# Performance work log

Measured on AMD Instinct MI355X. Metric: run time of the kernel, lower is better.

Reference implementation:

```python
import jax, jax.numpy as jnp
import numpy as np

B, C, T = 256, 1, 16384   # batch, input_channels, seq_len
H = C                      # hidden_size == input_channels in this module
OUT = 1                    # output_channels


def setup_inputs() -> dict:
    key = jax.random.key(0)
    ks = jax.random.split(key, 11)
    # PyTorch GRU/Linear init: uniform(-1/sqrt(H), 1/sqrt(H)); H=1 -> (-1, 1)
    u = lambda k, shape, s=1.0: jax.random.uniform(k, shape, jnp.float32, -s, s)
    s_lin = 1.0 / np.sqrt(2 * H).astype(np.float32)
    return {
        "x": jax.random.normal(ks[0], (B, C, T), jnp.float32),
        # layer 0: input size C, per direction [3H, C] / [3H, H] / [3H]
        "w_ih0": u(ks[1], (2, 3 * H, C)),
        "w_hh0": u(ks[2], (2, 3 * H, H)),
        "b_ih0": u(ks[3], (2, 3 * H)),
        "b_hh0": u(ks[4], (2, 3 * H)),
        # layers 1-2: input size 2H (bidirectional concat)
        "w_ih12": u(ks[5], (2, 2, 3 * H, 2 * H)),
        "w_hh12": u(ks[6], (2, 2, 3 * H, H)),
        "b_ih12": u(ks[7], (2, 2, 3 * H)),
        "b_hh12": u(ks[8], (2, 2, 3 * H)),
        # output projection Linear(2H -> OUT)
        "w_out": u(ks[9], (OUT, 2 * H), s_lin),
        "b_out": u(ks[10], (OUT,), s_lin),
    }


def _gru_dir(xs, w_ih, w_hh, b_ih, b_hh, reverse):
    """One GRU direction. xs: [T, B, in] -> ys: [T, B, H] (time-aligned)."""
    h0 = jnp.zeros((xs.shape[1], w_hh.shape[1]), xs.dtype)

    def step(h, x_t):
        gi = x_t @ w_ih.T + b_ih          # [B, 3H]
        gh = h @ w_hh.T + b_hh            # [B, 3H]
        ir, iz, inn = jnp.split(gi, 3, axis=-1)
        hr, hz, hn = jnp.split(gh, 3, axis=-1)
        r = jax.nn.sigmoid(ir + hr)
        z = jax.nn.sigmoid(iz + hz)
        n = jnp.tanh(inn + r * hn)
        h_new = (1.0 - z) * n + z * h
        return h_new, h_new

    _, ys = jax.lax.scan(step, h0, xs, reverse=reverse)
    return ys


def _bidir(xs, w_ih_f, w_hh_f, b_ih_f, b_hh_f, w_ih_b, w_hh_b, b_ih_b, b_hh_b):
    fwd = _gru_dir(xs, w_ih_f, w_hh_f, b_ih_f, b_hh_f, reverse=False)
    bwd = _gru_dir(xs, w_ih_b, w_hh_b, b_ih_b, b_hh_b, reverse=True)
    return jnp.concatenate([fwd, bwd], axis=-1)  # [T, B, 2H]


def reference(x, w_ih0, w_hh0, b_ih0, b_hh0, w_ih12, w_hh12, b_ih12, b_hh12, w_out, b_out):
    xs = jnp.transpose(x, (2, 0, 1))  # [B, C, T] -> [T, B, C]
    xs = _bidir(xs, w_ih0[0], w_hh0[0], b_ih0[0], b_hh0[0],
                w_ih0[1], w_hh0[1], b_ih0[1], b_hh0[1])
    for l in range(2):  # GRU layers 1 and 2 (structurally distinct weights)
        xs = _bidir(xs, w_ih12[l, 0], w_hh12[l, 0], b_ih12[l, 0], b_hh12[l, 0],
                    w_ih12[l, 1], w_hh12[l, 1], b_ih12[l, 1], b_hh12[l, 1])
    y = xs @ w_out.T + b_out          # [T, B, OUT]
    return jnp.transpose(y, (1, 2, 0))  # [B, OUT, T]
```

## Files before the change

### kernel.cpp

```cpp
#include <hip/hip_runtime.h>
#include <hip/hip_fp16.h>

#define T_LEN 16384
#define B_SZ  256
#define S_CH  256
#define CL    (T_LEN / S_CH)
#define HALO  32
#define SC    16

__device__ __forceinline__ float ex2(float x)  { return __builtin_amdgcn_exp2f(x); }
__device__ __forceinline__ float rcpf(float x) { return __builtin_amdgcn_rcpf(x); }

__device__ __forceinline__ float ld_cvt(const float* p)  { return *p; }
__device__ __forceinline__ float ld_cvt(const __half* p) { return __half2float(*p); }
__device__ __forceinline__ void  st_cvt(float* p, float v)  { *p = v; }
__device__ __forceinline__ void  st_cvt(__half* p, float v) { *p = __float2half_rn(v); }

__device__ __forceinline__ float gru_step(float h, float preR, float preZ, float preN,
                                          float UR, float UZ, float UN2, float DN2)
{
    float er  = ex2(fmaf(h, UR, preR));
    float ez  = ex2(fmaf(h, UZ, preZ));
    float r   = rcpf(1.0f + er);
    float z   = rcpf(1.0f + ez);
    float hn2 = fmaf(h, UN2, DN2);
    float en  = ex2(fmaf(r, hn2, preN));
    float n   = fmaf(-2.0f, rcpf(1.0f + en), 1.0f);
    float omz = 1.0f - z;
    float zh  = z * h;
    return fmaf(n, omz, zh);
}

template<bool REV>
__device__ void scan0(const float* __restrict__ x,
                      const float* __restrict__ wih, const float* __restrict__ whh,
                      const float* __restrict__ bih, const float* __restrict__ bhh,
                      __half* __restrict__ out, int b, int s)
{
    const int d = REV ? 1 : 0;
    const float L2E = 1.4426950408889634f;
    const float WR  = -L2E * wih[d*3+0];
    const float WZ  = -L2E * wih[d*3+1];
    const float WN  =  2.0f*L2E * wih[d*3+2];
    const float UR  = -L2E * whh[d*3+0];
    const float UZ  = -L2E * whh[d*3+1];
    const float UN2 =  2.0f*L2E * whh[d*3+2];
    const float CR  = -L2E * (bih[d*3+0] + bhh[d*3+0]);
    const float CZ  = -L2E * (bih[d*3+1] + bhh[d*3+1]);
    const float CN  =  2.0f*L2E * bih[d*3+2];
    const float DN2 =  2.0f*L2E * bhh[d*3+2];

    const int warm   = min(HALO, REV ? (T_LEN - (s + 1) * CL) : (s * CL));
    const int nsteps = warm + CL;
    const int t0     = REV ? ((s + 1) * CL - 1 + warm) : (s * CL - warm);

    const float* row = x + (size_t)b * T_LEN;
    __half* po = out + (REV ? B_SZ : 0) + b;

    float xA[SC], xB[SC];
    float h = 0.0f;

    auto LD = [&](float* F, int base) {
        const float4* p = (const float4*)(row + (REV ? (t0 - base - 15) : (t0 + base)));
        float4 v0 = p[0], v1 = p[1], v2 = p[2], v3 = p[3];
        float lin[16] = { v0.x,v0.y,v0.z,v0.w, v1.x,v1.y,v1.z,v1.w,
                          v2.x,v2.y,v2.z,v2.w, v3.x,v3.y,v3.z,v3.w };
        #pragma unroll
        for (int k = 0; k < 16; ++k) F[k] = REV ? lin[15 - k] : lin[k];
        __builtin_amdgcn_sched_barrier(0);
    };

    auto CS = [&](float* F, int base) {
        float ov[SC];
        #pragma unroll
        for (int k = 0; k < SC; ++k) {
            float xv = F[k];
            h = gru_step(h, fmaf(xv, WR, CR), fmaf(xv, WZ, CZ), fmaf(xv, WN, CN),
                         UR, UZ, UN2, DN2);
            ov[k] = h;
        }
        if (base >= warm) {
            #pragma unroll
            for (int k = 0; k < SC; ++k) {
                int t = REV ? (t0 - (base + k)) : (t0 + (base + k));
                st_cvt(po + t * (2 * B_SZ), ov[k]);
            }
        }
    };

    LD(xA, 0);
    const int nsup = nsteps / SC;
    for (int i = 0; i < nsup; i += 2) {
        LD(xB, min((i + 1) * SC, nsteps - SC));
        CS(xA, i * SC);
        LD(xA, min((i + 2) * SC, nsteps - SC));
        CS(xB, (i + 1) * SC);
    }
}

template<bool REV, typename TIN, typename TOUT>
__device__ void scan12(const TIN* __restrict__ in,
                       const float* __restrict__ wih, const float* __restrict__ whh,
                       const float* __restrict__ bih, const float* __restrict__ bhh,
                       TOUT* __restrict__ out, int b, int s)
{
    const int d = REV ? 1 : 0;
    const float L2E = 1.4426950408889634f;
    const float WR0 = -L2E * wih[(d*3+0)*2+0], WR1 = -L2E * wih[(d*3+0)*2+1];
    const float WZ0 = -L2E * wih[(d*3+1)*2+0], WZ1 = -L2E * wih[(d*3+1)*2+1];
    const float WN0 =  2.0f*L2E * wih[(d*3+2)*2+0], WN1 = 2.0f*L2E * wih[(d*3+2)*2+1];
    const float UR  = -L2E * whh[d*3+0];
    const float UZ  = -L2E * whh[d*3+1];
    const float UN2 =  2.0f*L2E * whh[d*3+2];
    const float CR  = -L2E * (bih[d*3+0] + bhh[d*3+0]);
    const float CZ  = -L2E * (bih[d*3+1] + bhh[d*3+1]);
    const float CN  =  2.0f*L2E * bih[d*3+2];
    const float DN2 =  2.0f*L2E * bhh[d*3+2];

    const int warm   = min(HALO, REV ? (T_LEN - (s + 1) * CL) : (s * CL));
    const int nsteps = warm + CL;
    const int t0     = REV ? ((s + 1) * CL - 1 + warm) : (s * CL - warm);

    const TIN* pf = in + b;
    const TIN* pg = in + B_SZ + b;
    TOUT* po = out + (REV ? B_SZ : 0) + b;

    float fA[SC], gA[SC], fB[SC], gB[SC];
    float h = 0.0f;

#define LD12(F, G, base_) { int base = (base_); \
    _Pragma("unroll") for (int k = 0; k < SC; ++k) { \
      int t = REV ? (t0 - (base + k)) : (t0 + (base + k)); \
      F[k] = ld_cvt(pf + t * (2 * B_SZ)); G[k] = ld_cvt(pg + t * (2 * B_SZ)); } \
    __builtin_amdgcn_sched_barrier(0); }

#define CS12(F, G, base_) { int base = (base_); float ov[SC]; \
    _Pragma("unroll") for (int k = 0; k < SC; ++k) { \
      float a = F[k], c = G[k]; \
      float pr = fmaf(a, WR0, fmaf(c, WR1, CR)); \
      float pz = fmaf(a, WZ0, fmaf(c, WZ1, CZ)); \
      float pn = fmaf(a, WN0, fmaf(c, WN1, CN)); \
      h = gru_step(h, pr, pz, pn, UR, UZ, UN2, DN2); ov[k] = h; } \
    if (base >= warm) { \
      _Pragma("unroll") for (int k = 0; k < SC; ++k) { \
        int t = REV ? (t0 - (base + k)) : (t0 + (base + k)); \
        st_cvt(po + t * (2 * B_SZ), ov[k]); } } }

    LD12(fA, gA, 0);
    const int nsup = nsteps / SC;
    for (int i = 0; i < nsup; i += 2) {
        LD12(fB, gB, min((i + 1) * SC, nsteps - SC));
        CS12(fA, gA, i * SC);
        LD12(fA, gA, min((i + 2) * SC, nsteps - SC));
        CS12(fB, gB, (i + 1) * SC);
    }
#undef LD12
#undef CS12
}

__device__ __forceinline__ void decode_blk(int blk, int tid, int& b, int& s, int& dir)
{
    int xcd = blk & 7;
    int j   = blk >> 3;
    int sl  = j & 31;
    int bg  = (j >> 5) & 3;
    dir     = j >> 7;
    s       = xcd * 32 + sl;
    b       = bg * 64 + tid;
}

__global__ void __launch_bounds__(64) k_scan0g(const float* __restrict__ x,
                                               const float* __restrict__ wih,
                                               const float* __restrict__ whh,
                                               const float* __restrict__ bih,
                                               const float* __restrict__ bhh,
                                               __half* __restrict__ out)
{
    int b, s, dir;
    decode_blk(blockIdx.x, threadIdx.x, b, s, dir);
    if (dir == 0) scan0<false>(x, wih, whh, bih, bhh, out, b, s);
    else          scan0<true >(x, wih, whh, bih, bhh, out, b, s);
}

__global__ void __launch_bounds__(64) k_scan1g(const __half* __restrict__ in,
                                               const float* __restrict__ wih,
                                               const float* __restrict__ whh,
                                               const float* __restrict__ bih,
                                               const float* __restrict__ bhh,
                                               __half* __restrict__ out)
{
    int b, s, dir;
    decode_blk(blockIdx.x, threadIdx.x, b, s, dir);
    if (dir == 0) scan12<false>(in, wih, whh, bih, bhh, out, b, s);
    else          scan12<true >(in, wih, whh, bih, bhh, out, b, s);
}

__global__ void __launch_bounds__(128) k2p(const __half* __restrict__ in,
        const float* __restrict__ wih, const float* __restrict__ whh,
        const float* __restrict__ bih, const float* __restrict__ bhh,
        const float* __restrict__ wo, const float* __restrict__ bo,
        float* __restrict__ y)
{
    __shared__ float tY[64][65];

    const int blk  = blockIdx.x;
    const int xcd  = blk & 7;
    const int jj   = blk >> 3;
    const int sl   = jj & 31;
    const int bg   = jj >> 5;
    const int s    = xcd * 32 + sl;
    const int lane = threadIdx.x & 63;
    const int w    = threadIdx.x >> 6;
    const int b    = bg * 64 + lane;
    const int sg   = w ? -1 : 1;
    const int t0   = s * CL;

    const int d = w;
    const float L2E = 1.4426950408889634f;
    const float WR0 = -L2E * wih[(d*3+0)*2+0], WR1 = -L2E * wih[(d*3+0)*2+1];
    const float WZ0 = -L2E * wih[(d*3+1)*2+0], WZ1 = -L2E * wih[(d*3+1)*2+1];
    const float WN0 =  2.0f*L2E * wih[(d*3+2)*2+0], WN1 = 2.0f*L2E * wih[(d*3+2)*2+1];
    const float UR  = -L2E * whh[d*3+0];
    const float UZ  = -L2E * whh[d*3+1];
    const float UN2 =  2.0f*L2E * whh[d*3+2];
    const float CR  = -L2E * (bih[d*3+0] + bhh[d*3+0]);
    const float CZ  = -L2E * (bih[d*3+1] + bhh[d*3+1]);
    const float CN  =  2.0f*L2E * bih[d*3+2];
    const float DN2 =  2.0f*L2E * bhh[d*3+2];

    const int warm   = w ? min(HALO, T_LEN - (t0 + CL)) : min(HALO, t0);
    const int tstart = w ? (t0 + CL - 1 + warm) : (t0 - warm);

    const __half* pf = in + b;
    const __half* pg = in + B_SZ + b;

    float fA[SC], gA[SC], fB[SC], gB[SC];
    float f[CL];
    float h = 0.0f;

#define LD2(F, G, base_) { int base = (base_); \
    _Pragma("unroll") for (int k = 0; k < SC; ++k) { \
      int t = tstart + sg * (base + k); \
      F[k] = __half2float(pf[t * (2 * B_SZ)]); \
      G[k] = __half2float(pg[t * (2 * B_SZ)]); } \
    __builtin_amdgcn_sched_barrier(0); }

#define CSB(F, G) { \
    _Pragma("unroll") for (int k = 0; k < SC; ++k) { \
      float a = F[k], c = G[k]; \
      float pr = fmaf(a, WR0, fmaf(c, WR1, CR)); \
      float pz = fmaf(a, WZ0, fmaf(c, WZ1, CZ)); \
      float pn = fmaf(a, WN0, fmaf(c, WN1, CN)); \
      h = gru_step(h, pr, pz, pn, UR, UZ, UN2, DN2); } }

#define CSS(F, G, Q) { \
    _Pragma("unroll") for (int k = 0; k < SC; ++k) { \
      float a = F[k], c = G[k]; \
      float pr = fmaf(a, WR0, fmaf(c, WR1, CR)); \
      float pz = fmaf(a, WZ0, fmaf(c, WZ1, CZ)); \
      float pn = fmaf(a, WN0, fmaf(c, WN1, CN)); \
      h = gru_step(h, pr, pz, pn, UR, UZ, UN2, DN2); \
      f[(Q) * SC + k] = h; } }

    LD2(fA, gA, 0);
    if (warm) {
        LD2(fB, gB, SC);      CSB(fA, gA);
        LD2(fA, gA, 2 * SC);  CSB(fB, gB);
    }
    LD2(fB, gB, warm + SC);      CSS(fA, gA, 0);
    LD2(fA, gA, warm + 2 * SC);  CSS(fB, gB, 1);
    LD2(fB, gB, warm + 3 * SC);  CSS(fA, gA, 2);
                                 CSS(fB, gB, 3);
#undef LD2
#undef CSB
#undef CSS

    const float wf = wo[0], wb = wo[1], bias = bo[0];
    if (w == 0) {
        #pragma unroll
        for (int m = 0; m < CL; ++m) tY[lane][m] = fmaf(wf, f[m], bias);
    }
    __syncthreads();
    if (w == 1) {
        #pragma unroll
        for (int m = 0; m < CL; ++m) tY[lane][CL - 1 - m] += wb * f[m];
    }
    __syncthreads();
    {
        const int b0 = bg * 64;
        const int c4 = threadIdx.x & 15;
        const int r  = (threadIdx.x >> 4) & 7;
        #pragma unroll
        for (int i = 0; i < 8; ++i) {
            int brow = r + 8 * i;
            float4 v = make_float4(tY[brow][c4*4+0], tY[brow][c4*4+1],
                                   tY[brow][c4*4+2], tY[brow][c4*4+3]);
            ((float4*)y)[(size_t)(b0 + brow) * (T_LEN / 4) + (t0 >> 2) + c4] = v;
        }
    }
}

extern "C" void kernel_launch(void* const* d_in, const int* in_sizes, int n_in,
                              void* d_out, int out_size, void* d_ws, size_t ws_size,
                              hipStream_t stream)
{
    (void)in_sizes; (void)n_in; (void)out_size; (void)ws_size;
    const float* x      = (const float*)d_in[0];
    const float* w_ih0  = (const float*)d_in[1];
    const float* w_hh0  = (const float*)d_in[2];
    const float* b_ih0  = (const float*)d_in[3];
    const float* b_hh0  = (const float*)d_in[4];
    const float* w_ih12 = (const float*)d_in[5];
    const float* w_hh12 = (const float*)d_in[6];
    const float* b_ih12 = (const float*)d_in[7];
    const float* b_hh12 = (const float*)d_in[8];
    const float* w_out  = (const float*)d_in[9];
    const float* b_out  = (const float*)d_in[10];
    float* y = (float*)d_out;

    char* ws = (char*)d_ws;
    const size_t NN = (size_t)2 * B_SZ * T_LEN;
    __half* l0out = (__half*)ws;
    __half* l1out = (__half*)(ws + NN * 2);

    const int nblk = 8 * S_CH;
    k_scan0g<<<nblk, 64, 0, stream>>>(x,     w_ih0,       w_hh0,      b_ih0,      b_hh0,      l0out);
    k_scan1g<<<nblk, 64, 0, stream>>>(l0out, w_ih12 + 0,  w_hh12 + 0, b_ih12 + 0, b_hh12 + 0, l1out);
    k2p    <<<4 * S_CH, 128, 0, stream>>>(l1out, w_ih12 + 12, w_hh12 + 6, b_ih12 + 6, b_hh12 + 6,
                                          w_out, b_out, y);
}
```

Baseline: 143.1 us.

## Fuse all three GRU layers into one cooperative kernel with neighbor flags

Replaces the three-kernel sequence with one cooperatively launched kernel that runs layer 0, layer 1 and layer 2 plus the projection back to back. Between layers it waits only on the neighboring chunk's completion flag, not on a full grid barrier, so launch gaps and global serialization between layers go away. It needs a memset of the flags and full grid residency. The new fallback path splits layer 2 and the projection into separate kernels with an fp32 intermediate.

```diff
diff --git a/kernel.cpp b/kernel.cpp
--- a/kernel.cpp
+++ b/kernel.cpp
@@ -195,10 +195,59 @@
     else          scan12<true >(in, wih, whh, bih, bhh, out, b, s);
 }
 
-__global__ void __launch_bounds__(128) k2p(const __half* __restrict__ in,
-        const float* __restrict__ wih, const float* __restrict__ whh,
-        const float* __restrict__ bih, const float* __restrict__ bhh,
+__global__ void __launch_bounds__(64) k_scan2g(const __half* __restrict__ in,
+                                               const float* __restrict__ wih,
+                                               const float* __restrict__ whh,
+                                               const float* __restrict__ bih,
+                                               const float* __restrict__ bhh,
+                                               float* __restrict__ out)
+{
+    int b, s, dir;
+    decode_blk(blockIdx.x, threadIdx.x, b, s, dir);
+    if (dir == 0) scan12<false>(in, wih, whh, bih, bhh, out, b, s);
+    else          scan12<true >(in, wih, whh, bih, bhh, out, b, s);
+}
+
+__global__ void __launch_bounds__(256) k_proj(const float* __restrict__ h2,
+                                              const float* __restrict__ wo,
+                                              const float* __restrict__ bo,
+                                              float* __restrict__ y)
+{
+    __shared__ float tile[64][65];
+    const int b0 = (blockIdx.x & 3) * 64;
+    const int t0 = (blockIdx.x >> 2) * 64;
+    const float wf = wo[0], wb = wo[1], bias = bo[0];
+    const int bl = threadIdx.x & 63;
+    const int tg = threadIdx.x >> 6;
+    #pragma unroll
+    for (int i = 0; i < 16; ++i) {
+        int tl = tg * 16 + i;
+        int t  = t0 + tl;
+        float f = h2[(size_t)t * (2 * B_SZ) + b0 + bl];
+        float g = h2[(size_t)t * (2 * B_SZ) + B_SZ + b0 + bl];
+        tile[bl][tl] = fmaf(wf, f, fmaf(wb, g, bias));
+    }
+    __syncthreads();
+    const int c4 = threadIdx.x & 15;
+    const int r  = threadIdx.x >> 4;
+    #pragma unroll
+    for (int i = 0; i < 4; ++i) {
+        int brow = r + 16 * i;
+        float4 v = make_float4(tile[brow][c4*4+0], tile[brow][c4*4+1],
+                               tile[brow][c4*4+2], tile[brow][c4*4+3]);
+        ((float4*)y)[(size_t)(b0 + brow) * (T_LEN / 4) + t0 / 4 + c4] = v;
+    }
+}
+
+__global__ void __launch_bounds__(128, 2) k_fused(
+        const float* __restrict__ x,
+        const float* __restrict__ w_ih0, const float* __restrict__ w_hh0,
+        const float* __restrict__ b_ih0, const float* __restrict__ b_hh0,
+        const float* __restrict__ w_ih12, const float* __restrict__ w_hh12,
+        const float* __restrict__ b_ih12, const float* __restrict__ b_hh12,
         const float* __restrict__ wo, const float* __restrict__ bo,
+        __half* __restrict__ l0out, __half* __restrict__ l1out,
+        int* __restrict__ flagA, int* __restrict__ flagB,
         float* __restrict__ y)
 {
     __shared__ float tY[64][65];
@@ -215,28 +264,67 @@
     const int sg   = w ? -1 : 1;
     const int t0   = s * CL;
 
-    const int d = w;
-    const float L2E = 1.4426950408889634f;
-    const float WR0 = -L2E * wih[(d*3+0)*2+0], WR1 = -L2E * wih[(d*3+0)*2+1];
-    const float WZ0 = -L2E * wih[(d*3+1)*2+0], WZ1 = -L2E * wih[(d*3+1)*2+1];
-    const float WN0 =  2.0f*L2E * wih[(d*3+2)*2+0], WN1 = 2.0f*L2E * wih[(d*3+2)*2+1];
-    const float UR  = -L2E * whh[d*3+0];
-    const float UZ  = -L2E * whh[d*3+1];
-    const float UN2 =  2.0f*L2E * whh[d*3+2];
-    const float CR  = -L2E * (bih[d*3+0] + bhh[d*3+0]);
-    const float CZ  = -L2E * (bih[d*3+1] + bhh[d*3+1]);
-    const float CN  =  2.0f*L2E * bih[d*3+2];
-    const float DN2 =  2.0f*L2E * bhh[d*3+2];
-
-    const int warm   = w ? min(HALO, T_LEN - (t0 + CL)) : min(HALO, t0);
-    const int tstart = w ? (t0 + CL - 1 + warm) : (t0 - warm);
-
-    const __half* pf = in + b;
-    const __half* pg = in + B_SZ + b;
-
-    float fA[SC], gA[SC], fB[SC], gB[SC];
-    float f[CL];
-    float h = 0.0f;
+    if (w == 0) scan0<false>(x, w_ih0, w_hh0, b_ih0, b_hh0, l0out, b, s);
+    else        scan0<true >(x, w_ih0, w_hh0, b_ih0, b_hh0, l0out, b, s);
+
+    __syncthreads();
+    if (threadIdx.x == 0)
+        __hip_atomic_store(&flagA[bg * S_CH + s], 1, __ATOMIC_RELEASE,
+                           __HIP_MEMORY_SCOPE_AGENT);
+    {
+        int nb = w ? (s + 1) : (s - 1);
+        if (nb >= 0 && nb < S_CH) {
+            const int* p = &flagA[bg * S_CH + nb];
+            while (__hip_atomic_load(p, __ATOMIC_ACQUIRE,
+                                     __HIP_MEMORY_SCOPE_AGENT) == 0)
+                __builtin_amdgcn_s_sleep(4);
+        }
+    }
+
+    if (w == 0) scan12<false>(l0out, w_ih12, w_hh12, b_ih12, b_hh12, l1out, b, s);
+    else        scan12<true >(l0out, w_ih12, w_hh12, b_ih12, b_hh12, l1out, b, s);
+
+    __syncthreads();
+    if (threadIdx.x == 0)
+        __hip_atomic_store(&flagB[bg * S_CH + s], 1, __ATOMIC_RELEASE,
+                           __HIP_MEMORY_SCOPE_AGENT);
+    {
+        int nb = w ? (s + 1) : (s - 1);
+        if (nb >= 0 && nb < S_CH) {
+            const int* p = &flagB[bg * S_CH + nb];
+            while (__hip_atomic_load(p, __ATOMIC_ACQUIRE,
+                                     __HIP_MEMORY_SCOPE_AGENT) == 0)
+                __builtin_amdgcn_s_sleep(4);
+        }
+    }
+
+    {
+        const float* wih = w_ih12 + 12;
+        const float* whh = w_hh12 + 6;
+        const float* bih = b_ih12 + 6;
+        const float* bhh = b_hh12 + 6;
+        const int d = w;
+        const float L2E = 1.4426950408889634f;
+        const float WR0 = -L2E * wih[(d*3+0)*2+0], WR1 = -L2E * wih[(d*3+0)*2+1];
+        const float WZ0 = -L2E * wih[(d*3+1)*2+0], WZ1 = -L2E * wih[(d*3+1)*2+1];
+        const float WN0 =  2.0f*L2E * wih[(d*3+2)*2+0], WN1 = 2.0f*L2E * wih[(d*3+2)*2+1];
+        const float UR  = -L2E * whh[d*3+0];
+        const float UZ  = -L2E * whh[d*3+1];
+        const float UN2 =  2.0f*L2E * whh[d*3+2];
+        const float CR  = -L2E * (bih[d*3+0] + bhh[d*3+0]);
+        const float CZ  = -L2E * (bih[d*3+1] + bhh[d*3+1]);
+        const float CN  =  2.0f*L2E * bih[d*3+2];
+        const float DN2 =  2.0f*L2E * bhh[d*3+2];
+
+        const int warm   = w ? min(HALO, T_LEN - (t0 + CL)) : min(HALO, t0);
+        const int tstart = w ? (t0 + CL - 1 + warm) : (t0 - warm);
+
+        const __half* pf = l1out + b;
+        const __half* pg = l1out + B_SZ + b;
+
+        float fA[SC], gA[SC], fB[SC], gB[SC];
+        float f[CL];
+        float h = 0.0f;
 
 #define LD2(F, G, base_) { int base = (base_); \
     _Pragma("unroll") for (int k = 0; k < SC; ++k) { \
@@ -262,40 +350,41 @@
       h = gru_step(h, pr, pz, pn, UR, UZ, UN2, DN2); \
       f[(Q) * SC + k] = h; } }
 
-    LD2(fA, gA, 0);
-    if (warm) {
-        LD2(fB, gB, SC);      CSB(fA, gA);
-        LD2(fA, gA, 2 * SC);  CSB(fB, gB);
-    }
-    LD2(fB, gB, warm + SC);      CSS(fA, gA, 0);
-    LD2(fA, gA, warm + 2 * SC);  CSS(fB, gB, 1);
-    LD2(fB, gB, warm + 3 * SC);  CSS(fA, gA, 2);
-                                 CSS(fB, gB, 3);
+        LD2(fA, gA, 0);
+        if (warm) {
+            LD2(fB, gB, SC);      CSB(fA, gA);
+            LD2(fA, gA, 2 * SC);  CSB(fB, gB);
+        }
+        LD2(fB, gB, warm + SC);      CSS(fA, gA, 0);
+        LD2(fA, gA, warm + 2 * SC);  CSS(fB, gB, 1);
+        LD2(fB, gB, warm + 3 * SC);  CSS(fA, gA, 2);
+                                     CSS(fB, gB, 3);
 #undef LD2
 #undef CSB
 #undef CSS
 
-    const float wf = wo[0], wb = wo[1], bias = bo[0];
-    if (w == 0) {
-        #pragma unroll
-        for (int m = 0; m < CL; ++m) tY[lane][m] = fmaf(wf, f[m], bias);
-    }
-    __syncthreads();
-    if (w == 1) {
-        #pragma unroll
-        for (int m = 0; m < CL; ++m) tY[lane][CL - 1 - m] += wb * f[m];
-    }
-    __syncthreads();
-    {
-        const int b0 = bg * 64;
-        const int c4 = threadIdx.x & 15;
-        const int r  = (threadIdx.x >> 4) & 7;
-        #pragma unroll
-        for (int i = 0; i < 8; ++i) {
-            int brow = r + 8 * i;
-            float4 v = make_float4(tY[brow][c4*4+0], tY[brow][c4*4+1],
-                                   tY[brow][c4*4+2], tY[brow][c4*4+3]);
-            ((float4*)y)[(size_t)(b0 + brow) * (T_LEN / 4) + (t0 >> 2) + c4] = v;
+        const float wf = wo[0], wb = wo[1], bias = bo[0];
+        if (w == 0) {
+            #pragma unroll
+            for (int m = 0; m < CL; ++m) tY[lane][m] = fmaf(wf, f[m], bias);
+        }
+        __syncthreads();
+        if (w == 1) {
+            #pragma unroll
+            for (int m = 0; m < CL; ++m) tY[lane][CL - 1 - m] += wb * f[m];
+        }
+        __syncthreads();
+        {
+            const int b0 = bg * 64;
+            const int c4 = threadIdx.x & 15;
+            const int r  = (threadIdx.x >> 4) & 7;
+            #pragma unroll
+            for (int i = 0; i < 8; ++i) {
+                int brow = r + 8 * i;
+                float4 v = make_float4(tY[brow][c4*4+0], tY[brow][c4*4+1],
+                                       tY[brow][c4*4+2], tY[brow][c4*4+3]);
+                ((float4*)y)[(size_t)(b0 + brow) * (T_LEN / 4) + (t0 >> 2) + c4] = v;
+            }
         }
     }
 }
@@ -322,10 +411,36 @@
     const size_t NN = (size_t)2 * B_SZ * T_LEN;
     __half* l0out = (__half*)ws;
     __half* l1out = (__half*)(ws + NN * 2);
+    float*  l2out = (float*)(ws + NN * 4);
+    int*    flagA = (int*)(ws + NN * 8);
+    int*    flagB = flagA + 4 * S_CH;
+
+    static int use_coop = -1;
+    if (use_coop < 0) {
+        int mab = 0;
+        hipError_t e = hipOccupancyMaxActiveBlocksPerMultiprocessor(&mab, k_fused, 128, 0);
+        use_coop = (e == hipSuccess && mab * 256 >= 4 * S_CH) ? 1 : 0;
+    }
+
+    if (use_coop) {
+        hipMemsetAsync(flagA, 0, 8 * S_CH * sizeof(int), stream);
+        void* args[] = { (void*)&x,
+                         (void*)&w_ih0, (void*)&w_hh0, (void*)&b_ih0, (void*)&b_hh0,
+                         (void*)&w_ih12, (void*)&w_hh12, (void*)&b_ih12, (void*)&b_hh12,
+                         (void*)&w_out, (void*)&b_out,
+                         (void*)&l0out, (void*)&l1out,
+                         (void*)&flagA, (void*)&flagB,
+                         (void*)&y };
+        hipError_t e = hipLaunchCooperativeKernel((const void*)k_fused,
+                                                  dim3(4 * S_CH), dim3(128),
+                                                  args, 0u, stream);
+        if (e == hipSuccess) return;
+        use_coop = 0;
+    }
 
     const int nblk = 8 * S_CH;
     k_scan0g<<<nblk, 64, 0, stream>>>(x,     w_ih0,       w_hh0,      b_ih0,      b_hh0,      l0out);
     k_scan1g<<<nblk, 64, 0, stream>>>(l0out, w_ih12 + 0,  w_hh12 + 0, b_ih12 + 0, b_hh12 + 0, l1out);
-    k2p    <<<4 * S_CH, 128, 0, stream>>>(l1out, w_ih12 + 12, w_hh12 + 6, b_ih12 + 6, b_hh12 + 6,
-                                          w_out, b_out, y);
-}
+    k_scan2g<<<nblk, 64, 0, stream>>>(l1out, w_ih12 + 12, w_hh12 + 6, b_ih12 + 6, b_hh12 + 6, l2out);
+    k_proj  <<<1024, 256, 0, stream>>>(l2out, w_out, b_out, y);
+}
```

New measurement: 139.2 us. -2.7%, faster.

## Fuse all three GRU layers into one kernel with LDS intermediates

Applied to the files above, without the earlier changes.

Replaces the three-kernel pipeline with a single kernel. Each block runs layer 0 and layer 1 over a widened time window (extra halos) and keeps their half-precision outputs in LDS instead of global workspace, then runs layer 2 and the output projection. This removes global round-trips of the intermediate activations and two kernel launches. In exchange, every block redoes more warm-up recurrence steps, and the 80KB of LDS per block limits how many blocks can share a CU, which reduces latency hiding for the serial scan.

```diff
diff --git a/kernel.cpp b/kernel.cpp
--- a/kernel.cpp
+++ b/kernel.cpp
@@ -10,11 +10,6 @@
 
 __device__ __forceinline__ float ex2(float x)  { return __builtin_amdgcn_exp2f(x); }
 __device__ __forceinline__ float rcpf(float x) { return __builtin_amdgcn_rcpf(x); }
-
-__device__ __forceinline__ float ld_cvt(const float* p)  { return *p; }
-__device__ __forceinline__ float ld_cvt(const __half* p) { return __half2float(*p); }
-__device__ __forceinline__ void  st_cvt(float* p, float v)  { *p = v; }
-__device__ __forceinline__ void  st_cvt(__half* p, float v) { *p = __float2half_rn(v); }
 
 __device__ __forceinline__ float gru_step(float h, float preR, float preZ, float preN,
                                           float UR, float UZ, float UN2, float DN2)
@@ -32,10 +27,10 @@
 }
 
 template<bool REV>
-__device__ void scan0(const float* __restrict__ x,
-                      const float* __restrict__ wih, const float* __restrict__ whh,
-                      const float* __restrict__ bih, const float* __restrict__ bhh,
-                      __half* __restrict__ out, int b, int s)
+__device__ __forceinline__ void stageA(const float* __restrict__ x,
+        const float* __restrict__ wih, const float* __restrict__ whh,
+        const float* __restrict__ bih, const float* __restrict__ bhh,
+        __half* __restrict__ l0h, int lane, int b, int a0, int e0)
 {
     const int d = REV ? 1 : 0;
     const float L2E = 1.4426950408889634f;
@@ -50,18 +45,16 @@
     const float CN  =  2.0f*L2E * bih[d*3+2];
     const float DN2 =  2.0f*L2E * bhh[d*3+2];
 
-    const int warm   = min(HALO, REV ? (T_LEN - (s + 1) * CL) : (s * CL));
-    const int nsteps = warm + CL;
-    const int t0     = REV ? ((s + 1) * CL - 1 + warm) : (s * CL - warm);
-
+    const int warm = REV ? min(HALO, T_LEN - e0) : min(HALO, a0);
+    const int nst  = warm + (e0 - a0);
+    const int ts   = REV ? (e0 - 1 + warm) : (a0 - warm);
     const float* row = x + (size_t)b * T_LEN;
-    __half* po = out + (REV ? B_SZ : 0) + b;
 
     float xA[SC], xB[SC];
     float h = 0.0f;
 
     auto LD = [&](float* F, int base) {
-        const float4* p = (const float4*)(row + (REV ? (t0 - base - 15) : (t0 + base)));
+        const float4* p = (const float4*)(row + (REV ? (ts - base - 15) : (ts + base)));
         float4 v0 = p[0], v1 = p[1], v2 = p[2], v3 = p[3];
         float lin[16] = { v0.x,v0.y,v0.z,v0.w, v1.x,v1.y,v1.z,v1.w,
                           v2.x,v2.y,v2.z,v2.w, v3.x,v3.y,v3.z,v3.w };
@@ -82,27 +75,27 @@
         if (base >= warm) {
             #pragma unroll
             for (int k = 0; k < SC; ++k) {
-                int t = REV ? (t0 - (base + k)) : (t0 + (base + k));
-                st_cvt(po + t * (2 * B_SZ), ov[k]);
+                int t = REV ? (ts - (base + k)) : (ts + (base + k));
+                l0h[((t - a0) * 64 + lane) * 2 + d] = __float2half_rn(ov[k]);
             }
         }
     };
 
     LD(xA, 0);
-    const int nsup = nsteps / SC;
+    const int nsup = nst / SC;
     for (int i = 0; i < nsup; i += 2) {
-        LD(xB, min((i + 1) * SC, nsteps - SC));
+        LD(xB, min((i + 1) * SC, nst - SC));
         CS(xA, i * SC);
-        LD(xA, min((i + 2) * SC, nsteps - SC));
+        LD(xA, min((i + 2) * SC, nst - SC));
         CS(xB, (i + 1) * SC);
     }
 }
 
-template<bool REV, typename TIN, typename TOUT>
-__device__ void scan12(const TIN* __restrict__ in,
-                       const float* __restrict__ wih, const float* __restrict__ whh,
-                       const float* __restrict__ bih, const float* __restrict__ bhh,
-                       TOUT* __restrict__ out, int b, int s)
+template<bool REV>
+__device__ __forceinline__ void stageB(const __half* __restrict__ l0h,
+        const float* __restrict__ wih, const float* __restrict__ whh,
+        const float* __restrict__ bih, const float* __restrict__ bhh,
+        __half* __restrict__ l1h, int lane, int a0, int a1, int e1)
 {
     const int d = REV ? 1 : 0;
     const float L2E = 1.4426950408889634f;
@@ -117,24 +110,22 @@
     const float CN  =  2.0f*L2E * bih[d*3+2];
     const float DN2 =  2.0f*L2E * bhh[d*3+2];
 
-    const int warm   = min(HALO, REV ? (T_LEN - (s + 1) * CL) : (s * CL));
-    const int nsteps = warm + CL;
-    const int t0     = REV ? ((s + 1) * CL - 1 + warm) : (s * CL - warm);
-
-    const TIN* pf = in + b;
-    const TIN* pg = in + B_SZ + b;
-    TOUT* po = out + (REV ? B_SZ : 0) + b;
+    const int warm = REV ? min(HALO, T_LEN - e1) : min(HALO, a1);
+    const int nst  = warm + (e1 - a1);
+    const int ts   = REV ? (e1 - 1 + warm) : (a1 - warm);
+    const __half2* src = (const __half2*)l0h;
 
     float fA[SC], gA[SC], fB[SC], gB[SC];
     float h = 0.0f;
 
-#define LD12(F, G, base_) { int base = (base_); \
-    _Pragma("unroll") for (int k = 0; k < SC; ++k) { \
-      int t = REV ? (t0 - (base + k)) : (t0 + (base + k)); \
-      F[k] = ld_cvt(pf + t * (2 * B_SZ)); G[k] = ld_cvt(pg + t * (2 * B_SZ)); } \
+#define LDB(F, G, base_) { int base = (base_); \
+    _Pragma("unroll") for (int k = 0; k < SC; ++k) { \
+      int t = REV ? (ts - (base + k)) : (ts + (base + k)); \
+      __half2 v = src[(t - a0) * 64 + lane]; \
+      F[k] = __low2float(v); G[k] = __high2float(v); } \
     __builtin_amdgcn_sched_barrier(0); }
 
-#define CS12(F, G, base_) { int base = (base_); float ov[SC]; \
+#define CSB12(F, G, base_) { int base = (base_); float ov[SC]; \
     _Pragma("unroll") for (int k = 0; k < SC; ++k) { \
       float a = F[k], c = G[k]; \
       float pr = fmaf(a, WR0, fmaf(c, WR1, CR)); \
@@ -143,65 +134,33 @@
       h = gru_step(h, pr, pz, pn, UR, UZ, UN2, DN2); ov[k] = h; } \
     if (base >= warm) { \
       _Pragma("unroll") for (int k = 0; k < SC; ++k) { \
-        int t = REV ? (t0 - (base + k)) : (t0 + (base + k)); \
-        st_cvt(po + t * (2 * B_SZ), ov[k]); } } }
-
-    LD12(fA, gA, 0);
-    const int nsup = nsteps / SC;
+        int t = REV ? (ts - (base + k)) : (ts + (base + k)); \
+        l1h[((t - a1) * 64 + lane) * 2 + d] = __float2half_rn(ov[k]); } } }
+
+    LDB(fA, gA, 0);
+    const int nsup = nst / SC;
     for (int i = 0; i < nsup; i += 2) {
-        LD12(fB, gB, min((i + 1) * SC, nsteps - SC));
-        CS12(fA, gA, i * SC);
-        LD12(fA, gA, min((i + 2) * SC, nsteps - SC));
-        CS12(fB, gB, (i + 1) * SC);
+        LDB(fB, gB, min((i + 1) * SC, nst - SC));
+        CSB12(fA, gA, i * SC);
+        LDB(fA, gA, min((i + 2) * SC, nst - SC));
+        CSB12(fB, gB, (i + 1) * SC);
     }
-#undef LD12
-#undef CS12
-}
-
-__device__ __forceinline__ void decode_blk(int blk, int tid, int& b, int& s, int& dir)
-{
-    int xcd = blk & 7;
-    int j   = blk >> 3;
-    int sl  = j & 31;
-    int bg  = (j >> 5) & 3;
-    dir     = j >> 7;
-    s       = xcd * 32 + sl;
-    b       = bg * 64 + tid;
-}
-
-__global__ void __launch_bounds__(64) k_scan0g(const float* __restrict__ x,
-                                               const float* __restrict__ wih,
-                                               const float* __restrict__ whh,
-                                               const float* __restrict__ bih,
-                                               const float* __restrict__ bhh,
-                                               __half* __restrict__ out)
-{
-    int b, s, dir;
-    decode_blk(blockIdx.x, threadIdx.x, b, s, dir);
-    if (dir == 0) scan0<false>(x, wih, whh, bih, bhh, out, b, s);
-    else          scan0<true >(x, wih, whh, bih, bhh, out, b, s);
-}
-
-__global__ void __launch_bounds__(64) k_scan1g(const __half* __restrict__ in,
-                                               const float* __restrict__ wih,
-                                               const float* __restrict__ whh,
-                                               const float* __restrict__ bih,
-                                               const float* __restrict__ bhh,
-                                               __half* __restrict__ out)
-{
-    int b, s, dir;
-    decode_blk(blockIdx.x, threadIdx.x, b, s, dir);
-    if (dir == 0) scan12<false>(in, wih, whh, bih, bhh, out, b, s);
-    else          scan12<true >(in, wih, whh, bih, bhh, out, b, s);
-}
-
-__global__ void __launch_bounds__(128) k2p(const __half* __restrict__ in,
-        const float* __restrict__ wih, const float* __restrict__ whh,
-        const float* __restrict__ bih, const float* __restrict__ bhh,
+#undef LDB
+#undef CSB12
+}
+
+__global__ void __launch_bounds__(128) k_all(const float* __restrict__ x,
+        const float* __restrict__ w_ih0, const float* __restrict__ w_hh0,
+        const float* __restrict__ b_ih0, const float* __restrict__ b_hh0,
+        const float* __restrict__ w_ih12, const float* __restrict__ w_hh12,
+        const float* __restrict__ b_ih12, const float* __restrict__ b_hh12,
         const float* __restrict__ wo, const float* __restrict__ bo,
         float* __restrict__ y)
 {
-    __shared__ float tY[64][65];
+    __shared__ __align__(16) char smem[81920];
+    __half* l0h = (__half*)smem;
+    __half* l1h = (__half*)(smem + 49152);
+    float (*tY)[65] = (float(*)[65])smem;
 
     const int blk  = blockIdx.x;
     const int xcd  = blk & 7;
@@ -215,34 +174,52 @@
     const int sg   = w ? -1 : 1;
     const int t0   = s * CL;
 
-    const int d = w;
-    const float L2E = 1.4426950408889634f;
-    const float WR0 = -L2E * wih[(d*3+0)*2+0], WR1 = -L2E * wih[(d*3+0)*2+1];
-    const float WZ0 = -L2E * wih[(d*3+1)*2+0], WZ1 = -L2E * wih[(d*3+1)*2+1];
-    const float WN0 =  2.0f*L2E * wih[(d*3+2)*2+0], WN1 = 2.0f*L2E * wih[(d*3+2)*2+1];
-    const float UR  = -L2E * whh[d*3+0];
-    const float UZ  = -L2E * whh[d*3+1];
-    const float UN2 =  2.0f*L2E * whh[d*3+2];
-    const float CR  = -L2E * (bih[d*3+0] + bhh[d*3+0]);
-    const float CZ  = -L2E * (bih[d*3+1] + bhh[d*3+1]);
-    const float CN  =  2.0f*L2E * bih[d*3+2];
-    const float DN2 =  2.0f*L2E * bhh[d*3+2];
-
-    const int warm   = w ? min(HALO, T_LEN - (t0 + CL)) : min(HALO, t0);
-    const int tstart = w ? (t0 + CL - 1 + warm) : (t0 - warm);
-
-    const __half* pf = in + b;
-    const __half* pg = in + B_SZ + b;
-
-    float fA[SC], gA[SC], fB[SC], gB[SC];
-    float f[CL];
-    float h = 0.0f;
+    const int WCf = min(HALO, t0);
+    const int WCb = min(HALO, T_LEN - (t0 + CL));
+    const int a1  = t0 - WCf, e1 = t0 + CL + WCb;
+    const int WBf = min(HALO, a1);
+    const int WBb = min(HALO, T_LEN - e1);
+    const int a0  = a1 - WBf, e0 = e1 + WBb;
+
+    if (w == 0) stageA<false>(x, w_ih0, w_hh0, b_ih0, b_hh0, l0h, lane, b, a0, e0);
+    else        stageA<true >(x, w_ih0, w_hh0, b_ih0, b_hh0, l0h, lane, b, a0, e0);
+    __syncthreads();
+
+    if (w == 0) stageB<false>(l0h, w_ih12, w_hh12, b_ih12, b_hh12, l1h, lane, a0, a1, e1);
+    else        stageB<true >(l0h, w_ih12, w_hh12, b_ih12, b_hh12, l1h, lane, a0, a1, e1);
+    __syncthreads();
+
+    {
+        const float* wih = w_ih12 + 12;
+        const float* whh = w_hh12 + 6;
+        const float* bih = b_ih12 + 6;
+        const float* bhh = b_hh12 + 6;
+        const int d = w;
+        const float L2E = 1.4426950408889634f;
+        const float WR0 = -L2E * wih[(d*3+0)*2+0], WR1 = -L2E * wih[(d*3+0)*2+1];
+        const float WZ0 = -L2E * wih[(d*3+1)*2+0], WZ1 = -L2E * wih[(d*3+1)*2+1];
+        const float WN0 =  2.0f*L2E * wih[(d*3+2)*2+0], WN1 = 2.0f*L2E * wih[(d*3+2)*2+1];
+        const float UR  = -L2E * whh[d*3+0];
+        const float UZ  = -L2E * whh[d*3+1];
+        const float UN2 =  2.0f*L2E * whh[d*3+2];
+        const float CR  = -L2E * (bih[d*3+0] + bhh[d*3+0]);
+        const float CZ  = -L2E * (bih[d*3+1] + bhh[d*3+1]);
+        const float CN  =  2.0f*L2E * bih[d*3+2];
+        const float DN2 =  2.0f*L2E * bhh[d*3+2];
+
+        const int warm   = w ? WCb : WCf;
+        const int tstart = w ? (e1 - 1) : a1;
+        const __half2* src = (const __half2*)l1h;
+
+        float fA[SC], gA[SC], fB[SC], gB[SC];
+        float f[CL];
+        float h = 0.0f;
 
 #define LD2(F, G, base_) { int base = (base_); \
     _Pragma("unroll") for (int k = 0; k < SC; ++k) { \
       int t = tstart + sg * (base + k); \
-      F[k] = __half2float(pf[t * (2 * B_SZ)]); \
-      G[k] = __half2float(pg[t * (2 * B_SZ)]); } \
+      __half2 v = src[(t - a1) * 64 + lane]; \
+      F[k] = __low2float(v); G[k] = __high2float(v); } \
     __builtin_amdgcn_sched_barrier(0); }
 
 #define CSB(F, G) { \
@@ -262,40 +239,41 @@
       h = gru_step(h, pr, pz, pn, UR, UZ, UN2, DN2); \
       f[(Q) * SC + k] = h; } }
 
-    LD2(fA, gA, 0);
-    if (warm) {
-        LD2(fB, gB, SC);      CSB(fA, gA);
-        LD2(fA, gA, 2 * SC);  CSB(fB, gB);
-    }
-    LD2(fB, gB, warm + SC);      CSS(fA, gA, 0);
-    LD2(fA, gA, warm + 2 * SC);  CSS(fB, gB, 1);
-    LD2(fB, gB, warm + 3 * SC);  CSS(fA, gA, 2);
-                                 CSS(fB, gB, 3);
+        LD2(fA, gA, 0);
+        if (warm) {
+            LD2(fB, gB, SC);      CSB(fA, gA);
+            LD2(fA, gA, 2 * SC);  CSB(fB, gB);
+        }
+        LD2(fB, gB, warm + SC);      CSS(fA, gA, 0);
+        LD2(fA, gA, warm + 2 * SC);  CSS(fB, gB, 1);
+        LD2(fB, gB, warm + 3 * SC);  CSS(fA, gA, 2);
+                                     CSS(fB, gB, 3);
 #undef LD2
 #undef CSB
 #undef CSS
 
-    const float wf = wo[0], wb = wo[1], bias = bo[0];
-    if (w == 0) {
-        #pragma unroll
-        for (int m = 0; m < CL; ++m) tY[lane][m] = fmaf(wf, f[m], bias);
-    }
-    __syncthreads();
-    if (w == 1) {
-        #pragma unroll
-        for (int m = 0; m < CL; ++m) tY[lane][CL - 1 - m] += wb * f[m];
-    }
-    __syncthreads();
-    {
-        const int b0 = bg * 64;
-        const int c4 = threadIdx.x & 15;
-        const int r  = (threadIdx.x >> 4) & 7;
-        #pragma unroll
-        for (int i = 0; i < 8; ++i) {
-            int brow = r + 8 * i;
-            float4 v = make_float4(tY[brow][c4*4+0], tY[brow][c4*4+1],
-                                   tY[brow][c4*4+2], tY[brow][c4*4+3]);
-            ((float4*)y)[(size_t)(b0 + brow) * (T_LEN / 4) + (t0 >> 2) + c4] = v;
+        const float wf = wo[0], wb = wo[1], bias = bo[0];
+        if (w == 0) {
+            #pragma unroll
+            for (int m = 0; m < CL; ++m) tY[lane][m] = fmaf(wf, f[m], bias);
+        }
+        __syncthreads();
+        if (w == 1) {
+            #pragma unroll
+            for (int m = 0; m < CL; ++m) tY[lane][CL - 1 - m] += wb * f[m];
+        }
+        __syncthreads();
+        {
+            const int b0 = bg * 64;
+            const int c4 = threadIdx.x & 15;
+            const int r  = (threadIdx.x >> 4) & 7;
+            #pragma unroll
+            for (int i = 0; i < 8; ++i) {
+                int brow = r + 8 * i;
+                float4 v = make_float4(tY[brow][c4*4+0], tY[brow][c4*4+1],
+                                       tY[brow][c4*4+2], tY[brow][c4*4+3]);
+                ((float4*)y)[(size_t)(b0 + brow) * (T_LEN / 4) + (t0 >> 2) + c4] = v;
+            }
         }
     }
 }
@@ -304,7 +282,7 @@
                               void* d_out, int out_size, void* d_ws, size_t ws_size,
                               hipStream_t stream)
 {
-    (void)in_sizes; (void)n_in; (void)out_size; (void)ws_size;
+    (void)in_sizes; (void)n_in; (void)out_size; (void)d_ws; (void)ws_size;
     const float* x      = (const float*)d_in[0];
     const float* w_ih0  = (const float*)d_in[1];
     const float* w_hh0  = (const float*)d_in[2];
@@ -318,14 +296,7 @@
     const float* b_out  = (const float*)d_in[10];
     float* y = (float*)d_out;
 
-    char* ws = (char*)d_ws;
-    const size_t NN = (size_t)2 * B_SZ * T_LEN;
-    __half* l0out = (__half*)ws;
-    __half* l1out = (__half*)(ws + NN * 2);
-
-    const int nblk = 8 * S_CH;
-    k_scan0g<<<nblk, 64, 0, stream>>>(x,     w_ih0,       w_hh0,      b_ih0,      b_hh0,      l0out);
-    k_scan1g<<<nblk, 64, 0, stream>>>(l0out, w_ih12 + 0,  w_hh12 + 0, b_ih12 + 0, b_hh12 + 0, l1out);
-    k2p    <<<4 * S_CH, 128, 0, stream>>>(l1out, w_ih12 + 12, w_hh12 + 6, b_ih12 + 6, b_hh12 + 6,
-                                          w_out, b_out, y);
-}
+    k_all<<<4 * S_CH, 128, 0, stream>>>(x, w_ih0, w_hh0, b_ih0, b_hh0,
+                                        w_ih12, w_hh12, b_ih12, b_hh12,
+                                        w_out, b_out, y);
+}
```

New measurement: 144.3 us. No clear change (+0.9%).
